# Kernel optimization log

Hardware: AMD Instinct MI355X
Metric: run time of the kernel (lower is better)

## Reference

```python
import jax, jax.numpy as jnp
import numpy as np

K = 32
TEMPERATURE = 0.1
RTOL, ATOL = 1e-5, 1e-5


def _embed(x, W1, b1, W2, b2, W3, b3):
    h = jax.nn.gelu(x @ W1.T + b1, approximate=False)
    h = jax.nn.gelu(h @ W2.T + b2, approximate=False)
    return jax.nn.sigmoid(h @ W3.T + b3)


def setup_inputs() -> dict:
    key = jax.random.key(0)
    ks = jax.random.split(key, 9)
    Q, N, D_IN, D_E = 256, 16384, 256, 64
    s = lambda fan_in: 1.0 / np.sqrt(fan_in)
    return {
        "x": jax.random.normal(ks[0], (Q, D_IN), jnp.float32),
        "support_x": jax.random.normal(ks[1], (N, D_IN), jnp.float32),
        "support_labels": jax.random.uniform(ks[2], (N, 1), jnp.float32),
        "W1": jax.random.normal(ks[3], (D_E, D_IN), jnp.float32) * s(D_IN),
        "b1": jax.random.normal(ks[4], (D_E,), jnp.float32) * s(D_IN),
        "W2": jax.random.normal(ks[5], (D_E, D_E), jnp.float32) * s(D_E),
        "b2": jax.random.normal(ks[6], (D_E,), jnp.float32) * s(D_E),
        "W3": jax.random.normal(ks[7], (D_E, D_E), jnp.float32) * s(D_E),
        "b3": jax.random.normal(ks[8], (D_E,), jnp.float32) * s(D_E),
    }


def reference(x, support_x, support_labels, W1, b1, W2, b2, W3, b3):
    # query embeddings [Q, D]; support embeddings [N, D] (set_support is no_grad)
    q = _embed(x, W1, b1, W2, b2, W3, b3)
    s = jax.lax.stop_gradient(_embed(support_x, W1, b1, W2, b2, W3, b3))
    # torch.cdist p=2 via expanded squared distances
    d2 = (jnp.sum(q * q, -1)[:, None] + jnp.sum(s * s, -1)[None, :]
          - 2.0 * (q @ s.T))
    dist = jnp.sqrt(jnp.maximum(d2, 0.0))  # [Q, N]
    # isclose mask: |q - s| <= atol + rtol*|s|, all over feature dim
    close = jnp.abs(q[:, None, :] - s[None, :, :]) <= (ATOL + RTOL * jnp.abs(s)[None, :, :])
    mask = jnp.all(close, axis=-1)  # [Q, N]
    dist = jnp.where(mask, jnp.inf, dist)
    # top-k smallest distances
    neg_top, idx = jax.lax.top_k(-dist, K)  # [Q, K]
    topd = -neg_top
    neighbor_labels = support_labels[idx].squeeze(-1)  # [Q, K]
    weights = jax.nn.softmax(-topd / TEMPERATURE, axis=1)
    return jnp.sum(weights * neighbor_labels, axis=1)  # [Q]
```

## Files before the change

### kernel.cpp

```cpp
#include <hip/hip_runtime.h>
#include <math.h>

#define D_IN   256
#define D_E    64
#define N_SUP  16384
#define NQ     256
#define KSEL   32
#define RTOLC  1e-5f
#define ATOLC  1e-5f
#define INV_T  10.0f

#define CHUNK  1024
#define NCH    16
#define QG     8
#define NQG    32

typedef unsigned long long ull;

__device__ __forceinline__ float gelu_exact(float x) {
    return 0.5f * x * (1.0f + erff(x * 0.70710678118654752440f));
}

__global__ __launch_bounds__(256) void prep_w(
    const float* __restrict__ W1, const float* __restrict__ W2,
    const float* __restrict__ W3,
    float* __restrict__ W1T, float* __restrict__ W2T, float* __restrict__ W3T)
{
    const int t = blockIdx.x * 256 + threadIdx.x;
    const int stride = gridDim.x * 256;
    for (int o = t; o < D_E * D_IN; o += stride) {
        int f = o >> 8, k = o & 255;
        W1T[k * D_E + f] = W1[o];
    }
    for (int o = t; o < D_E * D_E; o += stride) {
        int f = o >> 6, k = o & 63;
        W2T[k * D_E + f] = W2[o];
        W3T[k * D_E + f] = W3[o];
    }
}

__global__ __launch_bounds__(512, 6) void embed_kernel(
    const float* __restrict__ sx, const float* __restrict__ x,
    const float* __restrict__ W1T, const float* __restrict__ b1,
    const float* __restrict__ W2T, const float* __restrict__ b2,
    const float* __restrict__ W3T, const float* __restrict__ b3,
    float* __restrict__ s_emb, float* __restrict__ s_norm,
    float* __restrict__ q_emb, float* __restrict__ q_norm)
{
    __shared__ float xc[64][65];
    __shared__ float hA[64][65];
    __shared__ float hB[64][65];
    __shared__ float nsum[64][9];

    const int tid  = threadIdx.x;
    const int lane = tid & 63;
    const int wv   = tid >> 6;
    const int f0   = __builtin_amdgcn_readfirstlane(wv * 8);
    const bool isq = blockIdx.x >= (N_SUP / 64);
    const float* src = isq ? (x + (size_t)(blockIdx.x - N_SUP / 64) * 64 * D_IN)
                           : (sx + (size_t)blockIdx.x * 64 * D_IN);

    float acc[8];
    #pragma unroll
    for (int i = 0; i < 8; ++i) acc[i] = b1[f0 + i];

    for (int kc = 0; kc < 4; ++kc) {
        __syncthreads();
        #pragma unroll
        for (int i = 0; i < 2; ++i) {
            int g   = i * 512 + tid;
            int row = g >> 4;
            int c4  = g & 15;
            float4 v = *reinterpret_cast<const float4*>(
                src + (size_t)row * D_IN + kc * 64 + c4 * 4);
            xc[c4 * 4 + 0][row] = v.x; xc[c4 * 4 + 1][row] = v.y;
            xc[c4 * 4 + 2][row] = v.z; xc[c4 * 4 + 3][row] = v.w;
        }
        __syncthreads();
        const float* wbase = W1T + (size_t)(kc * 64) * D_E + f0;
        #pragma unroll 8
        for (int k = 0; k < 64; ++k) {
            float xk = xc[k][lane];
            const float* wk = wbase + k * D_E;
            #pragma unroll
            for (int f = 0; f < 8; ++f) acc[f] = fmaf(wk[f], xk, acc[f]);
        }
    }
    #pragma unroll
    for (int i = 0; i < 8; ++i) hA[f0 + i][lane] = gelu_exact(acc[i]);
    __syncthreads();

    float a2[8];
    #pragma unroll
    for (int i = 0; i < 8; ++i) a2[i] = b2[f0 + i];
    #pragma unroll 8
    for (int k = 0; k < D_E; ++k) {
        float hk = hA[k][lane];
        const float* wk = W2T + k * D_E + f0;
        #pragma unroll
        for (int f = 0; f < 8; ++f) a2[f] = fmaf(wk[f], hk, a2[f]);
    }
    #pragma unroll
    for (int i = 0; i < 8; ++i) hB[f0 + i][lane] = gelu_exact(a2[i]);
    __syncthreads();

    float a3[8];
    #pragma unroll
    for (int i = 0; i < 8; ++i) a3[i] = b3[f0 + i];
    #pragma unroll 8
    for (int k = 0; k < D_E; ++k) {
        float hk = hB[k][lane];
        const float* wk = W3T + k * D_E + f0;
        #pragma unroll
        for (int f = 0; f < 8; ++f) a3[f] = fmaf(wk[f], hk, a3[f]);
    }
    float e[8];
    float np = 0.0f;
    #pragma unroll
    for (int i = 0; i < 8; ++i) {
        e[i] = 1.0f / (1.0f + expf(-a3[i]));
        np = fmaf(e[i], e[i], np);
    }

    const int rowl = isq ? (blockIdx.x - N_SUP / 64) * 64 + lane
                         : blockIdx.x * 64 + lane;
    float* E   = isq ? q_emb  : s_emb;
    float* Nrm = isq ? q_norm : s_norm;
    float* erow = E + (size_t)rowl * D_E + f0;
    *reinterpret_cast<float4*>(erow)     = make_float4(e[0], e[1], e[2], e[3]);
    *reinterpret_cast<float4*>(erow + 4) = make_float4(e[4], e[5], e[6], e[7]);

    nsum[lane][wv] = np;
    __syncthreads();
    if (wv == 0) {
        float s = 0.0f;
        #pragma unroll
        for (int w = 0; w < 8; ++w) s += nsum[lane][w];
        Nrm[rowl] = s;
    }
}

__global__ __launch_bounds__(512, 4) void knn_phaseA(
    const float* __restrict__ s_emb, const float* __restrict__ s_norm,
    const float* __restrict__ q_emb, const float* __restrict__ q_norm,
    ull* __restrict__ cand)
{
    __shared__ float tile[128 * 68];
    __shared__ float d2l[QG][CHUNK];

    const int tid  = threadIdx.x;
    const int lane = tid & 63;
    const int wid  = tid >> 6;
    const int qg   = blockIdx.x >> 4;
    const int sc   = blockIdx.x & 15;

    const int qp = __builtin_amdgcn_readfirstlane(tid >> 7);
    const float* q0 = q_emb + (size_t)(qg * QG + 2 * qp) * D_E;
    const float* q1 = q0 + D_E;
    const float qn0 = q_norm[qg * QG + 2 * qp];
    const float qn1 = q_norm[qg * QG + 2 * qp + 1];
    const int rl = tid & 127;

    for (int s = 0; s < 8; ++s) {
        __syncthreads();
        #pragma unroll
        for (int i = 0; i < 4; ++i) {
            int g   = i * 512 + tid;
            int row = g >> 4, c4 = g & 15;
            float4 v = *reinterpret_cast<const float4*>(
                s_emb + (size_t)(sc * CHUNK + s * 128 + row) * D_E + c4 * 4);
            *reinterpret_cast<float4*>(&tile[row * 68 + c4 * 4]) = v;
        }
        __syncthreads();

        const float* tr = &tile[rl * 68];
        float a0 = 0.0f, a1 = 0.0f;
        #pragma unroll
        for (int c = 0; c < 16; ++c) {
            float4 sv = *reinterpret_cast<const float4*>(tr + c * 4);
            a0 = fmaf(q0[c * 4 + 0], sv.x, a0);
            a0 = fmaf(q0[c * 4 + 1], sv.y, a0);
            a0 = fmaf(q0[c * 4 + 2], sv.z, a0);
            a0 = fmaf(q0[c * 4 + 3], sv.w, a0);
            a1 = fmaf(q1[c * 4 + 0], sv.x, a1);
            a1 = fmaf(q1[c * 4 + 1], sv.y, a1);
            a1 = fmaf(q1[c * 4 + 2], sv.z, a1);
            a1 = fmaf(q1[c * 4 + 3], sv.w, a1);
        }
        const int grow = sc * CHUNK + s * 128 + rl;
        const float sn = s_norm[grow];
        float d20 = fmaxf(qn0 + sn - 2.0f * a0, 0.0f);
        float d21 = fmaxf(qn1 + sn - 2.0f * a1, 0.0f);
        if (d20 < 1e-2f) {
            bool close = true;
            for (int k = 0; k < D_E; ++k) {
                float sv = tr[k];
                close = close && (fabsf(q0[k] - sv) <= (ATOLC + RTOLC * fabsf(sv)));
            }
            if (close) d20 = INFINITY;
        }
        if (d21 < 1e-2f) {
            bool close = true;
            for (int k = 0; k < D_E; ++k) {
                float sv = tr[k];
                close = close && (fabsf(q1[k] - sv) <= (ATOLC + RTOLC * fabsf(sv)));
            }
            if (close) d21 = INFINITY;
        }
        d2l[2 * qp][s * 128 + rl]     = d20;
        d2l[2 * qp + 1][s * 128 + rl] = d21;
    }
    __syncthreads();

    float v[16];
    #pragma unroll
    for (int j = 0; j < 16; ++j) v[j] = d2l[wid][j * 64 + lane];

    float    lmin = v[0];
    unsigned lrow = (unsigned)lane;
    #pragma unroll
    for (int j = 1; j < 16; ++j) {
        bool b = v[j] < lmin;
        lmin = b ? v[j] : lmin;
        lrow = b ? (unsigned)(j * 64 + lane) : lrow;
    }
    ull lkey = ((ull)__float_as_uint(lmin) << 10) | (ull)lrow;
    unsigned kmask = 0;
    ull* dst = cand + ((size_t)(qg * QG + wid) * NCH + sc) * KSEL;

    for (int it = 0; it < KSEL; ++it) {
        ull m = lkey;
        #pragma unroll
        for (int off = 1; off < 64; off <<= 1) {
            ull o = __shfl_xor(m, off);
            m = o < m ? o : m;
        }
        if (lane == 0)
            dst[it] = ((m >> 10) << 32) | (ull)(unsigned)(sc * CHUNK + (unsigned)(m & 1023u));
        if (lkey == m) {
            kmask |= 1u << ((unsigned)(m & 1023u) >> 6);
            float    nm = INFINITY;
            unsigned nr = 1023u;
            #pragma unroll
            for (int j = 0; j < 16; ++j) {
                if (!((kmask >> j) & 1u)) {
                    bool b = v[j] < nm;
                    nm = b ? v[j] : nm;
                    nr = b ? (unsigned)(j * 64 + lane) : nr;
                }
            }
            lmin = nm; lrow = nr;
            lkey = ((ull)__float_as_uint(nm) << 10) | (ull)nr;
        }
    }
}

__global__ __launch_bounds__(256) void knn_phaseB(
    const ull* __restrict__ cand, const float* __restrict__ labels,
    float* __restrict__ out)
{
    const int lane = threadIdx.x & 63;
    const int wid  = threadIdx.x >> 6;
    const int q    = blockIdx.x * 4 + wid;

    const ull* lst = cand + ((size_t)q * NCH + (lane & 15)) * KSEL;
    int ptr = 0;
    ull cur = (lane < NCH) ? lst[0] : ~0ull;

    float d0 = 0.0f, sw = 0.0f, sl = 0.0f;
    for (int it = 0; it < KSEL; ++it) {
        ull m = cur;
        #pragma unroll
        for (int off = 1; off < 16; off <<= 1) {
            ull o = __shfl_xor(m, off);
            m = o < m ? o : m;
        }
        if (lane < NCH && cur == m) {
            ++ptr;
            cur = (ptr < KSEL) ? lst[ptr] : ~0ull;
        }
        if (lane == 0) {
            unsigned idx = (unsigned)(m & 0xffffffffu);
            float d = sqrtf(__uint_as_float((unsigned)(m >> 32)));
            if (it == 0) d0 = d;
            float w = expf((d0 - d) * INV_T);
            sw += w;
            sl += w * labels[idx < N_SUP ? idx : 0];
        }
    }
    if (lane == 0) out[q] = sl / sw;
}

extern "C" void kernel_launch(void* const* d_in, const int* in_sizes, int n_in,
                              void* d_out, int out_size, void* d_ws, size_t ws_size,
                              hipStream_t stream) {
    const float* x      = (const float*)d_in[0];
    const float* sx     = (const float*)d_in[1];
    const float* labels = (const float*)d_in[2];
    const float* W1     = (const float*)d_in[3];
    const float* b1     = (const float*)d_in[4];
    const float* W2     = (const float*)d_in[5];
    const float* b2     = (const float*)d_in[6];
    const float* W3     = (const float*)d_in[7];
    const float* b3     = (const float*)d_in[8];
    float* out = (float*)d_out;

    float* ws     = (float*)d_ws;
    float* s_emb  = ws;
    float* s_norm = s_emb + N_SUP * D_E;
    float* q_emb  = s_norm + N_SUP;
    float* q_norm = q_emb + NQ * D_E;
    float* W1T    = q_norm + NQ;
    float* W2T    = W1T + D_IN * D_E;
    float* W3T    = W2T + D_E * D_E;
    ull*   cand   = (ull*)(W3T + D_E * D_E);

    prep_w<<<32, 256, 0, stream>>>(W1, W2, W3, W1T, W2T, W3T);
    embed_kernel<<<(N_SUP + NQ) / 64, 512, 0, stream>>>(
        sx, x, W1T, b1, W2T, b2, W3T, b3, s_emb, s_norm, q_emb, q_norm);
    knn_phaseA<<<NQG * NCH, 512, 0, stream>>>(s_emb, s_norm, q_emb, q_norm, cand);
    knn_phaseB<<<NQ / 4, 256, 0, stream>>>(cand, labels, out);
}
```

Measured before the change: 107.0 us.

## Sort per-lane candidates with bitonic network and fold labels into candidate list

```diff
diff --git a/kernel.cpp b/kernel.cpp
--- a/kernel.cpp
+++ b/kernel.cpp
@@ -143,91 +143,87 @@
 __global__ __launch_bounds__(512, 4) void knn_phaseA(
     const float* __restrict__ s_emb, const float* __restrict__ s_norm,
     const float* __restrict__ q_emb, const float* __restrict__ q_norm,
-    ull* __restrict__ cand)
+    const float* __restrict__ labels, ull* __restrict__ cand)
 {
-    __shared__ float tile[128 * 68];
+    __shared__ float tile[64 * 68];
     __shared__ float d2l[QG][CHUNK];
+    __shared__ ull   win_l[QG][KSEL];
 
     const int tid  = threadIdx.x;
     const int lane = tid & 63;
     const int wid  = tid >> 6;
     const int qg   = blockIdx.x >> 4;
     const int sc   = blockIdx.x & 15;
-
-    const int qp = __builtin_amdgcn_readfirstlane(tid >> 7);
-    const float* q0 = q_emb + (size_t)(qg * QG + 2 * qp) * D_E;
-    const float* q1 = q0 + D_E;
-    const float qn0 = q_norm[qg * QG + 2 * qp];
-    const float qn1 = q_norm[qg * QG + 2 * qp + 1];
-    const int rl = tid & 127;
-
-    for (int s = 0; s < 8; ++s) {
+    const int qiu  = __builtin_amdgcn_readfirstlane(qg * QG + wid);
+
+    const float* q0 = q_emb + (size_t)qiu * D_E;
+    const float  qn = q_norm[qiu];
+
+    for (int s = 0; s < 16; ++s) {
         __syncthreads();
         #pragma unroll
-        for (int i = 0; i < 4; ++i) {
+        for (int i = 0; i < 2; ++i) {
             int g   = i * 512 + tid;
             int row = g >> 4, c4 = g & 15;
             float4 v = *reinterpret_cast<const float4*>(
-                s_emb + (size_t)(sc * CHUNK + s * 128 + row) * D_E + c4 * 4);
+                s_emb + (size_t)(sc * CHUNK + s * 64 + row) * D_E + c4 * 4);
             *reinterpret_cast<float4*>(&tile[row * 68 + c4 * 4]) = v;
         }
         __syncthreads();
 
-        const float* tr = &tile[rl * 68];
-        float a0 = 0.0f, a1 = 0.0f;
+        const float* tr = &tile[lane * 68];
+        float a = 0.0f;
         #pragma unroll
         for (int c = 0; c < 16; ++c) {
             float4 sv = *reinterpret_cast<const float4*>(tr + c * 4);
-            a0 = fmaf(q0[c * 4 + 0], sv.x, a0);
-            a0 = fmaf(q0[c * 4 + 1], sv.y, a0);
-            a0 = fmaf(q0[c * 4 + 2], sv.z, a0);
-            a0 = fmaf(q0[c * 4 + 3], sv.w, a0);
-            a1 = fmaf(q1[c * 4 + 0], sv.x, a1);
-            a1 = fmaf(q1[c * 4 + 1], sv.y, a1);
-            a1 = fmaf(q1[c * 4 + 2], sv.z, a1);
-            a1 = fmaf(q1[c * 4 + 3], sv.w, a1);
-        }
-        const int grow = sc * CHUNK + s * 128 + rl;
-        const float sn = s_norm[grow];
-        float d20 = fmaxf(qn0 + sn - 2.0f * a0, 0.0f);
-        float d21 = fmaxf(qn1 + sn - 2.0f * a1, 0.0f);
-        if (d20 < 1e-2f) {
+            a = fmaf(q0[c * 4 + 0], sv.x, a);
+            a = fmaf(q0[c * 4 + 1], sv.y, a);
+            a = fmaf(q0[c * 4 + 2], sv.z, a);
+            a = fmaf(q0[c * 4 + 3], sv.w, a);
+        }
+        const int grow = sc * CHUNK + s * 64 + lane;
+        float d2 = fmaxf(qn + s_norm[grow] - 2.0f * a, 0.0f);
+        if (d2 < 1e-3f) {
             bool close = true;
             for (int k = 0; k < D_E; ++k) {
                 float sv = tr[k];
                 close = close && (fabsf(q0[k] - sv) <= (ATOLC + RTOLC * fabsf(sv)));
             }
-            if (close) d20 = INFINITY;
-        }
-        if (d21 < 1e-2f) {
-            bool close = true;
-            for (int k = 0; k < D_E; ++k) {
-                float sv = tr[k];
-                close = close && (fabsf(q1[k] - sv) <= (ATOLC + RTOLC * fabsf(sv)));
+            if (close) d2 = INFINITY;
+        }
+        d2l[wid][s * 64 + lane] = d2;
+    }
+
+    ull sk[16];
+    #pragma unroll
+    for (int j = 0; j < 16; ++j) {
+        float d2 = d2l[wid][j * 64 + lane];
+        sk[j] = ((ull)__float_as_uint(d2) << 10) | (unsigned)(j * 64 + lane);
+    }
+
+    #pragma unroll
+    for (int k = 2; k <= 16; k <<= 1) {
+        #pragma unroll
+        for (int j = k >> 1; j > 0; j >>= 1) {
+            #pragma unroll
+            for (int i = 0; i < 16; ++i) {
+                int ixj = i ^ j;
+                if (ixj > i) {
+                    if ((i & k) == 0) {
+                        ull a_ = sk[i], b_ = sk[ixj];
+                        bool c_ = b_ < a_;
+                        sk[i] = c_ ? b_ : a_; sk[ixj] = c_ ? a_ : b_;
+                    } else {
+                        ull a_ = sk[i], b_ = sk[ixj];
+                        bool c_ = a_ < b_;
+                        sk[i] = c_ ? b_ : a_; sk[ixj] = c_ ? a_ : b_;
+                    }
+                }
             }
-            if (close) d21 = INFINITY;
-        }
-        d2l[2 * qp][s * 128 + rl]     = d20;
-        d2l[2 * qp + 1][s * 128 + rl] = d21;
-    }
-    __syncthreads();
-
-    float v[16];
-    #pragma unroll
-    for (int j = 0; j < 16; ++j) v[j] = d2l[wid][j * 64 + lane];
-
-    float    lmin = v[0];
-    unsigned lrow = (unsigned)lane;
-    #pragma unroll
-    for (int j = 1; j < 16; ++j) {
-        bool b = v[j] < lmin;
-        lmin = b ? v[j] : lmin;
-        lrow = b ? (unsigned)(j * 64 + lane) : lrow;
-    }
-    ull lkey = ((ull)__float_as_uint(lmin) << 10) | (ull)lrow;
-    unsigned kmask = 0;
-    ull* dst = cand + ((size_t)(qg * QG + wid) * NCH + sc) * KSEL;
-
+        }
+    }
+
+    ull lkey = sk[0];
     for (int it = 0; it < KSEL; ++it) {
         ull m = lkey;
         #pragma unroll
@@ -235,57 +231,60 @@
             ull o = __shfl_xor(m, off);
             m = o < m ? o : m;
         }
-        if (lane == 0)
-            dst[it] = ((m >> 10) << 32) | (ull)(unsigned)(sc * CHUNK + (unsigned)(m & 1023u));
+        if (lane == it) win_l[wid][it] = m;
         if (lkey == m) {
-            kmask |= 1u << ((unsigned)(m & 1023u) >> 6);
-            float    nm = INFINITY;
-            unsigned nr = 1023u;
             #pragma unroll
-            for (int j = 0; j < 16; ++j) {
-                if (!((kmask >> j) & 1u)) {
-                    bool b = v[j] < nm;
-                    nm = b ? v[j] : nm;
-                    nr = b ? (unsigned)(j * 64 + lane) : nr;
-                }
-            }
-            lmin = nm; lrow = nr;
-            lkey = ((ull)__float_as_uint(nm) << 10) | (ull)nr;
-        }
+            for (int j = 0; j < 15; ++j) sk[j] = sk[j + 1];
+            sk[15] = ~0ull;
+            lkey = sk[0];
+        }
+    }
+
+    if (lane < KSEL) {
+        ull m = win_l[wid][lane];
+        unsigned gidx = (unsigned)(sc * CHUNK) + (unsigned)(m & 1023u);
+        float lab = labels[gidx];
+        ull* dst = cand + ((size_t)qiu * NCH + sc) * KSEL;
+        dst[lane] = ((ull)(unsigned)(m >> 10) << 32) | (ull)__float_as_uint(lab);
     }
 }
 
 __global__ __launch_bounds__(256) void knn_phaseB(
-    const ull* __restrict__ cand, const float* __restrict__ labels,
-    float* __restrict__ out)
+    const ull* __restrict__ cand, float* __restrict__ out)
 {
     const int lane = threadIdx.x & 63;
     const int wid  = threadIdx.x >> 6;
     const int q    = blockIdx.x * 4 + wid;
 
+    const bool act = lane < NCH;
     const ull* lst = cand + ((size_t)q * NCH + (lane & 15)) * KSEL;
     int ptr = 0;
-    ull cur = (lane < NCH) ? lst[0] : ~0ull;
+    ull cur = act ? lst[0] : ~0ull;
 
     float d0 = 0.0f, sw = 0.0f, sl = 0.0f;
     for (int it = 0; it < KSEL; ++it) {
-        ull m = cur;
+        unsigned mv = (unsigned)(cur >> 32);
+        unsigned ml = (unsigned)cur;
         #pragma unroll
         for (int off = 1; off < 16; off <<= 1) {
-            ull o = __shfl_xor(m, off);
-            m = o < m ? o : m;
-        }
-        if (lane < NCH && cur == m) {
+            unsigned ov = __shfl_xor(mv, off);
+            unsigned ol = __shfl_xor(ml, off);
+            bool take = (ov < mv) || (ov == mv && (lane & off));
+            mv = take ? ov : mv;
+            ml = take ? ol : ml;
+        }
+        ull b = __ballot(act && (unsigned)(cur >> 32) == mv);
+        int wl = (int)(__ffsll((long long)b) - 1);
+        if (lane == wl) {
             ++ptr;
             cur = (ptr < KSEL) ? lst[ptr] : ~0ull;
         }
         if (lane == 0) {
-            unsigned idx = (unsigned)(m & 0xffffffffu);
-            float d = sqrtf(__uint_as_float((unsigned)(m >> 32)));
+            float d = sqrtf(__uint_as_float(mv));
             if (it == 0) d0 = d;
             float w = expf((d0 - d) * INV_T);
             sw += w;
-            sl += w * labels[idx < N_SUP ? idx : 0];
+            sl += w * __uint_as_float(ml);
         }
     }
     if (lane == 0) out[q] = sl / sw;
@@ -318,6 +317,7 @@
     prep_w<<<32, 256, 0, stream>>>(W1, W2, W3, W1T, W2T, W3T);
     embed_kernel<<<(N_SUP + NQ) / 64, 512, 0, stream>>>(
         sx, x, W1T, b1, W2T, b2, W3T, b3, s_emb, s_norm, q_emb, q_norm);
-    knn_phaseA<<<NQG * NCH, 512, 0, stream>>>(s_emb, s_norm, q_emb, q_norm, cand);
-    knn_phaseB<<<NQ / 4, 256, 0, stream>>>(cand, labels, out);
-}
+    knn_phaseA<<<NQG * NCH, 512, 0, stream>>>(s_emb, s_norm, q_emb, q_norm,
+                                              labels, cand);
+    knn_phaseB<<<NQ / 4, 256, 0, stream>>>(cand, out);
+}
```

New measurement: 101.6 us. -5.1%, faster.
